# Performance work log

Measured on AMD Instinct MI355X. Metric: run time of the kernel, lower is better.

The kernel has to match this reference:

```python
import jax, jax.numpy as jnp
import numpy as np

# Quantization / threshold constants (from init_kwargs)
AQI, AQF = 8, 8      # activation fixed-point: int/frac bits
NQI, NQF = 2, 8      # nonlinearity output fixed-point
TH_X = 0.1           # delta threshold on input
TH_H = 0.1           # delta threshold on hidden state


def _round_ste(x):
    # straight-through round (GradPreserveRoundTensor in the original util)
    return x + jax.lax.stop_gradient(jnp.round(x) - x)


def quantize(x, qi, qf):
    # util.quantize_tensor with quantize=1: fake-quantize to Q(qi).(qf) fixed point
    power = jnp.asarray(2.0 ** qf, x.dtype)
    clip_val = 2.0 ** (qi + qf - 1)
    return jnp.clip(_round_ste(x * power), -clip_val, clip_val - 1) / power


def setup_inputs() -> dict:
    key = jax.random.key(0)
    k0, k1, k2, k3, k4 = jax.random.split(key, 5)
    T, B, I, H = 512, 64, 512, 1024
    G = 4 * H
    return {
        "x": jax.random.normal(k0, (T, B, I), jnp.float32),
        "weight_ih": jax.random.normal(k1, (G, I), jnp.float32) / np.sqrt(I).astype(np.float32),
        "weight_hh": jax.random.normal(k2, (G, H), jnp.float32) / np.sqrt(H).astype(np.float32),
        "bias_ih": jax.random.normal(k3, (G,), jnp.float32) * 0.1,
        "bias_hh": jax.random.normal(k4, (G,), jnp.float32) * 0.1,
    }


def reference(x, weight_ih, weight_hh, bias_ih, bias_hh):
    T, B, I = x.shape
    H = weight_hh.shape[1]
    dt = x.dtype

    th_x_q = quantize(jnp.asarray(TH_X, dt), AQI, AQF)  # quantized threshold for delta mask
    th_h_q = quantize(jnp.asarray(TH_H, dt), AQI, AQF)

    xs = quantize(x, AQI, AQF)  # inputs quantized once up front

    # initial state (initialize_state with state=None)
    x_prev0 = jnp.zeros((B, I), dt)           # Q(zeros) == zeros
    h0 = jnp.zeros((B, H), dt)
    hp0 = jnp.zeros((B, H), dt)
    c0 = jnp.zeros((B, H), dt)
    m0 = jnp.zeros((B, 4 * H), dt) + bias_ih + bias_hh  # biases folded into m once
    reg0 = jnp.zeros((), dt)

    w_ih_t = weight_ih.T  # [I, 4H]
    w_hh_t = weight_hh.T  # [H, 4H]

    def step(carry, x_t):
        x_prev, h, h_prev, c, m, reg = carry
        dx = x_t - x_prev
        dh = h - h_prev
        dxa = jnp.abs(dx)
        dha = jnp.abs(dh)
        dx = jnp.where(dxa < th_x_q, jnp.asarray(0, dt), dx)   # masked_fill with quantized th
        dh = jnp.where(dha < th_h_q, jnp.asarray(0, dt), dh)
        x_prev = jnp.where(dxa >= TH_X, x_t, x_prev)           # state update with raw th (as in source)
        h_prev = jnp.where(dha >= TH_H, h, h_prev)
        reg = reg + jnp.sum(jnp.abs(dh))                       # l1 norm of masked delta_h

        m = dx @ w_ih_t + dh @ w_hh_t + m                      # delta-GEMM accumulated into m
        pre = quantize(m, AQI, AQF)
        p_i, p_f, p_g, p_o = jnp.split(pre, 4, axis=1)
        g_i = quantize(jax.nn.sigmoid(p_i), NQI, NQF)
        g_f = quantize(jax.nn.sigmoid(p_f), NQI, NQF)
        g_o = quantize(jax.nn.sigmoid(p_o), NQI, NQF)
        g_g = quantize(jnp.tanh(p_g), NQI, NQF)

        c_new = c * g_f + g_i * g_g
        q_c = quantize(c_new, AQI, AQF)
        c_tanh = quantize(jnp.tanh(q_c), NQI, NQF)
        h_new = quantize(g_o * c_tanh, AQI, AQF)
        return (x_prev, h_new, h_prev, q_c, m, reg), h_new

    (x_prev, h, h_prev, c, m, reg), out = jax.lax.scan(
        step, (x_prev0, h0, hp0, c0, m0, reg0), xs)

    # x_prev_out is padded to [B, max(I, H)] (zeros beyond input_size)
    x_prev_out = jnp.zeros((B, max(I, H)), dt).at[:, :I].set(x_prev)
    # state tensors stacked over layers (num_layers=1)
    state = (x_prev_out[None], h[None], h_prev[None], c[None], m[None])
    return (out, *state, reg.reshape(1))
```

## Files before the change

kernel.cpp:

```cpp
#include <hip/hip_runtime.h>
#include <hip/hip_fp16.h>
#include <stdint.h>

typedef unsigned short ushort_t;
typedef unsigned int uint_t;
typedef unsigned long long ull_t;
typedef _Float16 half8 __attribute__((ext_vector_type(8)));
typedef float f32x4 __attribute__((ext_vector_type(4)));

#define TSTEPS 512
#define BATCH  64
#define ISZ    512
#define HSZ    1024
#define GSZ    4096
#define NB     256
#define NTH    1024
#define DHFRAG 65536

static constexpr size_t OFF_XPREV = (size_t)TSTEPS * BATCH * HSZ;
static constexpr size_t OFF_H     = OFF_XPREV + (size_t)BATCH * 1024;
static constexpr size_t OFF_HP    = OFF_H  + (size_t)BATCH * HSZ;
static constexpr size_t OFF_C     = OFF_HP + (size_t)BATCH * HSZ;
static constexpr size_t OFF_M     = OFF_C  + (size_t)BATCH * HSZ;
static constexpr size_t OFF_REG   = OFF_M  + (size_t)BATCH * GSZ;

#define TH_RAW 0.1f
#define TH_QNT 0.1015625f

__device__ __forceinline__ float qA(float x) {
  float v = rintf(x * 256.0f);
  v = fminf(fmaxf(v, -32768.0f), 32767.0f);
  return v * 0.00390625f;
}
__device__ __forceinline__ float qN(float x) {
  float v = rintf(x * 256.0f);
  v = fminf(fmaxf(v, -512.0f), 511.0f);
  return v * 0.00390625f;
}
__device__ __forceinline__ float sigm(float x) { return 1.0f / (1.0f + expf(-x)); }

__global__ __launch_bounds__(256) void xscan_kernel(const float* __restrict__ x,
                                                    __half* __restrict__ dx16,
                                                    float* __restrict__ out_xprev) {
  const int gid = blockIdx.x * blockDim.x + threadIdx.x;
  float xp = 0.0f;
  #pragma unroll 8
  for (int t = 0; t < TSTEPS; t++) {
    float xq = qA(x[(size_t)t * (BATCH * ISZ) + gid]);
    float d  = xq - xp;
    float da = fabsf(d);
    dx16[(size_t)t * (BATCH * ISZ) + gid] = __float2half((da < TH_QNT) ? 0.0f : d);
    if (da >= TH_RAW) xp = xq;
  }
  const int b = gid >> 9;
  const int i = gid & 511;
  out_xprev[(size_t)b * 1024 + i]       = xp;
  out_xprev[(size_t)b * 1024 + 512 + i] = 0.0f;
}

__device__ __forceinline__ void gbar_arrive(int* flags, int e) {
  asm volatile("s_waitcnt vmcnt(0)" ::: "memory");
  __syncthreads();
  if (threadIdx.x == 0) {
    __hip_atomic_store(&flags[blockIdx.x], e, __ATOMIC_RELAXED, __HIP_MEMORY_SCOPE_AGENT);
  }
}
__device__ __forceinline__ void gbar_wait(int* flags, int e) {
  if (threadIdx.x < 64) {
    const ull_t* f64 = (const ull_t*)flags;
    const int l = threadIdx.x;
    bool done;
    do {
      ull_t a = __hip_atomic_load(f64 + l,      __ATOMIC_RELAXED, __HIP_MEMORY_SCOPE_AGENT);
      ull_t c = __hip_atomic_load(f64 + 64 + l, __ATOMIC_RELAXED, __HIP_MEMORY_SCOPE_AGENT);
      bool ok = ((int)a >= e) & ((int)(a >> 32) >= e) &
                ((int)c >= e) & ((int)(c >> 32) >= e);
      done = __all(ok);
      if (!done) __builtin_amdgcn_s_sleep(2);
    } while (!done);
  }
  __syncthreads();
}

__global__ __launch_bounds__(NTH, 4) void scan_kernel(
    const __half* __restrict__ dx16, const float* __restrict__ w_ih,
    const float* __restrict__ w_hh, const float* __restrict__ b_ih,
    const float* __restrict__ b_hh, float* __restrict__ out,
    __half* __restrict__ dh16, float* __restrict__ partials, int* flags) {
  __shared__ __align__(16) unsigned char dxbuf[2][65536];
  __shared__ float part[4][64][17];
  __shared__ float red[256];

  const int tid  = threadIdx.x;
  const int wid  = tid >> 6;
  const int lane = tid & 63;
  const int bt   = wid >> 2;
  const int kg   = wid & 3;
  const int lr   = lane & 15;
  const int lq   = lane >> 4;
  const int lkb  = lq * 16;
  const int jb   = (blockIdx.x & 7) * 32 + (blockIdx.x >> 3);

  const int wrow = jb * 4 + (lr & 3) + (lr >> 2) * HSZ;
  half8 wx[4], wh[8];
  #pragma unroll
  for (int kt = 0; kt < 4; ++kt) {
    const float* p = w_ih + (size_t)wrow * ISZ + kg * 128 + kt * 32 + lq * 8;
    half8 v;
    #pragma unroll
    for (int e = 0; e < 8; ++e) v[e] = (_Float16)p[e];
    wx[kt] = v;
  }
  #pragma unroll
  for (int kt = 0; kt < 8; ++kt) {
    const float* p = w_hh + (size_t)wrow * HSZ + kg * 256 + kt * 32 + lq * 8;
    half8 v;
    #pragma unroll
    for (int e = 0; e < 8; ++e) v[e] = (_Float16)p[e];
    wh[kt] = v;
  }

  const int jj = tid & 3;
  const int cb = tid >> 2;
  const int j  = jb * 4 + jj;
  const int g0 = j, g1 = j + HSZ, g2 = j + 2 * HSZ, g3 = j + 3 * HSZ;
  float m0 = 0.f, m1 = 0.f, m2 = 0.f, m3 = 0.f;
  float c = 0.0f, hp = 0.0f, h = 0.0f, regacc = 0.0f;
  if (tid < 256) {
    m0 = b_ih[g0] + b_hh[g0];
    m1 = b_ih[g1] + b_hh[g1];
    m2 = b_ih[g2] + b_hh[g2];
    m3 = b_ih[g3] + b_hh[g3];
  }
  const size_t dhcell2 = ((size_t)(jb >> 1) * 64 + cb) * 2 + (jb & 1);

  const int arow = bt * 16 + lr;
  const int akey = (arow & 7) << 4;
  const int kc0  = kg * 32 + lq;

  {
    const ull_t* __restrict__ sx = (const ull_t*)dx16;
    #pragma unroll
    for (int i = 0; i < 8; ++i) {
      ull_t v = sx[i * 1024 + tid];
      const int u = i * 1024 + tid;
      const int row = u >> 7, cc = u & 127;
      *(ull_t*)(&dxbuf[0][0] + row * 1024 + ((cc * 8) ^ ((row & 7) << 4))) = v;
    }
  }
  __syncthreads();

  f32x4 acc = {0.f, 0.f, 0.f, 0.f};
  {
    const unsigned char* xbase = &dxbuf[0][0] + arow * 1024;
    #pragma unroll
    for (int kt = 0; kt < 4; ++kt) {
      const int col = kg * 256 + kt * 64 + lkb;
      union { uint4 u; half8 hv; } U;
      U.u = *(const uint4*)(xbase + (col ^ akey));
      acc = __builtin_amdgcn_mfma_f32_16x16x32_f16(U.hv, wx[kt], acc, 0, 0, 0);
    }
  }

  for (int t = 0; t < TSTEPS; t++) {
    gbar_wait(flags, t);

    const ull_t* __restrict__ hb = (const ull_t*)(dh16 + (size_t)(t & 1) * DHFRAG);
    ull_t lo[8], hi[8];
    #pragma unroll
    for (int kt = 0; kt < 8; ++kt) {
      const size_t ci = ((size_t)(kc0 + kt * 4) * 64 + arow) * 2;
      lo[kt] = __hip_atomic_load(hb + ci,     __ATOMIC_RELAXED, __HIP_MEMORY_SCOPE_AGENT);
      hi[kt] = __hip_atomic_load(hb + ci + 1, __ATOMIC_RELAXED, __HIP_MEMORY_SCOPE_AGENT);
    }
    #pragma unroll
    for (int kt = 0; kt < 8; ++kt) {
      union { ull_t u[2]; half8 hv; } U;
      U.u[0] = lo[kt]; U.u[1] = hi[kt];
      acc = __builtin_amdgcn_mfma_f32_16x16x32_f16(U.hv, wh[kt], acc, 0, 0, 0);
    }

    #pragma unroll
    for (int r = 0; r < 4; ++r)
      part[kg][bt * 16 + lq * 4 + r][lr] = acc[r];
    __syncthreads();

    if (tid < 256) {
      float s0 = 0.f, s1 = 0.f, s2 = 0.f, s3 = 0.f;
      #pragma unroll
      for (int k2 = 0; k2 < 4; ++k2) {
        s0 += part[k2][cb][jj];
        s1 += part[k2][cb][4 + jj];
        s2 += part[k2][cb][8 + jj];
        s3 += part[k2][cb][12 + jj];
      }
      m0 += s0; m1 += s1; m2 += s2; m3 += s3;

      float pi = qA(m0), pf = qA(m1), pg = qA(m2), po = qA(m3);
      float gi = qN(sigm(pi));
      float gf = qN(sigm(pf));
      float gg = qN(tanhf(pg));
      float go = qN(sigm(po));
      float cn = c * gf + gi * gg;
      c = qA(cn);
      float ct = qN(tanhf(c));
      h = qA(go * ct);

      if (t < TSTEPS - 1) {
        float d  = h - hp;
        float da = fabsf(d);
        float dm = (da < TH_QNT) ? 0.0f : d;
        if (da >= TH_RAW) hp = h;
        regacc += fabsf(dm);
        ushort_t my = __half_as_ushort(__float2half(dm));
        int v1 = __shfl((int)my, lane + 1, 64);
        int v2 = __shfl((int)my, lane + 2, 64);
        int v3 = __shfl((int)my, lane + 3, 64);
        if (jj == 0) {
          ull_t dw = (ull_t)my | ((ull_t)(ushort_t)v1 << 16) |
                     ((ull_t)(ushort_t)v2 << 32) | ((ull_t)(ushort_t)v3 << 48);
          ull_t* dhw = (ull_t*)(dh16 + (size_t)((t + 1) & 1) * DHFRAG);
          __hip_atomic_store(dhw + dhcell2, dw,
                             __ATOMIC_RELAXED, __HIP_MEMORY_SCOPE_AGENT);
        }
      }
    }

    gbar_arrive(flags, t + 1);

    if (tid < 256)
      out[(size_t)t * (BATCH * HSZ) + (size_t)cb * HSZ + j] = h;

    if (t + 1 < TSTEPS) {
      {
        const ull_t* __restrict__ sx =
            (const ull_t*)(dx16 + (size_t)(t + 1) * (BATCH * ISZ));
        unsigned char* dst = &dxbuf[(t + 1) & 1][0];
        #pragma unroll
        for (int i = 0; i < 8; ++i) {
          ull_t v = sx[i * 1024 + tid];
          const int u = i * 1024 + tid;
          const int row = u >> 7, cc = u & 127;
          *(ull_t*)(dst + row * 1024 + ((cc * 8) ^ ((row & 7) << 4))) = v;
        }
      }
      __syncthreads();
      {
        acc = (f32x4){0.f, 0.f, 0.f, 0.f};
        const unsigned char* xbase = &dxbuf[(t + 1) & 1][0] + arow * 1024;
        #pragma unroll
        for (int kt = 0; kt < 4; ++kt) {
          const int col = kg * 256 + kt * 64 + lkb;
          union { uint4 u; half8 hv; } U;
          U.u = *(const uint4*)(xbase + (col ^ akey));
          acc = __builtin_amdgcn_mfma_f32_16x16x32_f16(U.hv, wx[kt], acc, 0, 0, 0);
        }
      }
    }
  }

  if (tid < 256) {
    out[OFF_H  + (size_t)cb * HSZ + j] = h;
    out[OFF_HP + (size_t)cb * HSZ + j] = hp;
    out[OFF_C  + (size_t)cb * HSZ + j] = c;
    out[OFF_M  + (size_t)cb * GSZ + g0] = m0;
    out[OFF_M  + (size_t)cb * GSZ + g1] = m1;
    out[OFF_M  + (size_t)cb * GSZ + g2] = m2;
    out[OFF_M  + (size_t)cb * GSZ + g3] = m3;
  }

  if (tid < 256) red[tid] = regacc;
  __syncthreads();
  for (int s = 128; s > 0; s >>= 1) {
    if (tid < s) red[tid] += red[tid + s];
    __syncthreads();
  }
  if (tid == 0)
    __hip_atomic_store(&partials[blockIdx.x], red[0], __ATOMIC_RELAXED, __HIP_MEMORY_SCOPE_AGENT);
  gbar_arrive(flags, TSTEPS + 1);
  gbar_wait(flags, TSTEPS + 1);
  if (blockIdx.x == 0) {
    if (tid < 256)
      red[tid] = __hip_atomic_load(&partials[tid], __ATOMIC_RELAXED, __HIP_MEMORY_SCOPE_AGENT);
    __syncthreads();
    for (int s = 128; s > 0; s >>= 1) {
      if (tid < s) red[tid] += red[tid + s];
      __syncthreads();
    }
    if (tid == 0) out[OFF_REG] = red[0];
  }
}

extern "C" void kernel_launch(void* const* d_in, const int* in_sizes, int n_in,
                              void* d_out, int out_size, void* d_ws, size_t ws_size,
                              hipStream_t stream) {
  const float* x    = (const float*)d_in[0];
  const float* w_ih = (const float*)d_in[1];
  const float* w_hh = (const float*)d_in[2];
  const float* b_ih = (const float*)d_in[3];
  const float* b_hh = (const float*)d_in[4];
  float* out = (float*)d_out;

  const size_t dx_elems = (size_t)TSTEPS * BATCH * ISZ;
  __half* dx16     = (__half*)d_ws;
  __half* dh16     = dx16 + dx_elems;
  float*  partials = (float*)(dh16 + 2 * (size_t)DHFRAG);
  int*    flags    = (int*)(partials + NB);
  size_t needed = (size_t)((char*)(flags + NB) - (char*)d_ws);
  if (ws_size < needed) return;

  (void)hipMemsetAsync(dh16, 0, 2 * (size_t)DHFRAG * sizeof(__half), stream);
  (void)hipMemsetAsync(flags, 0, NB * sizeof(int), stream);
  xscan_kernel<<<128, 256, 0, stream>>>(x, dx16, out + OFF_XPREV);
  scan_kernel<<<NB, NTH, 0, stream>>>(dx16, w_ih, w_hh, b_ih, b_hh, out,
                                      dh16, partials, flags);
}
```

Baseline: 2.898 ms.

## Replace global barrier with per-wave partial flag waits and restructure step schedule

Each wave now polls only the 64 producer flags for the k-slice of dh it consumes, instead of every block waiting for all 256 flags. Each block publishes its own flag after a vmcnt drain and a block barrier. The dx-GEMM part is moved after the wait and overlapped with the dh loads, and the next step's dx tile is staged before a trailing syncthreads. A separate flag array serves the final reduction barrier. The aim is to cut inter-block barrier latency on the recurrent critical path, at the risk of memory-ordering subtleties with relaxed atomics.

```diff
diff --git a/kernel.cpp b/kernel.cpp
--- a/kernel.cpp
+++ b/kernel.cpp
@@ -86,7 +86,8 @@
     const __half* __restrict__ dx16, const float* __restrict__ w_ih,
     const float* __restrict__ w_hh, const float* __restrict__ b_ih,
     const float* __restrict__ b_hh, float* __restrict__ out,
-    __half* __restrict__ dh16, float* __restrict__ partials, int* flags) {
+    __half* __restrict__ dh16, float* __restrict__ partials,
+    int* flags, int* flagsE) {
   __shared__ __align__(16) unsigned char dxbuf[2][65536];
   __shared__ float part[4][64][17];
   __shared__ float red[256];
@@ -137,6 +138,7 @@
   const int arow = bt * 16 + lr;
   const int akey = (arow & 7) << 4;
   const int kc0  = kg * 32 + lq;
+  const int fidx = kg * 32 + (lane & 31);
 
   {
     const ull_t* __restrict__ sx = (const ull_t*)dx16;
@@ -150,20 +152,17 @@
   }
   __syncthreads();
 
-  f32x4 acc = {0.f, 0.f, 0.f, 0.f};
-  {
-    const unsigned char* xbase = &dxbuf[0][0] + arow * 1024;
-    #pragma unroll
-    for (int kt = 0; kt < 4; ++kt) {
-      const int col = kg * 256 + kt * 64 + lkb;
-      union { uint4 u; half8 hv; } U;
-      U.u = *(const uint4*)(xbase + (col ^ akey));
-      acc = __builtin_amdgcn_mfma_f32_16x16x32_f16(U.hv, wx[kt], acc, 0, 0, 0);
-    }
-  }
-
   for (int t = 0; t < TSTEPS; t++) {
-    gbar_wait(flags, t);
+    {
+      const ull_t* f64 = (const ull_t*)flags;
+      bool done;
+      do {
+        ull_t v = __hip_atomic_load(f64 + fidx, __ATOMIC_RELAXED, __HIP_MEMORY_SCOPE_AGENT);
+        done = __all(((int)v >= t) & ((int)(v >> 32) >= t));
+        if (!done) __builtin_amdgcn_s_sleep(1);
+      } while (!done);
+      asm volatile("" ::: "memory");
+    }
 
     const ull_t* __restrict__ hb = (const ull_t*)(dh16 + (size_t)(t & 1) * DHFRAG);
     ull_t lo[8], hi[8];
@@ -172,6 +171,18 @@
       const size_t ci = ((size_t)(kc0 + kt * 4) * 64 + arow) * 2;
       lo[kt] = __hip_atomic_load(hb + ci,     __ATOMIC_RELAXED, __HIP_MEMORY_SCOPE_AGENT);
       hi[kt] = __hip_atomic_load(hb + ci + 1, __ATOMIC_RELAXED, __HIP_MEMORY_SCOPE_AGENT);
+    }
+
+    f32x4 acc = {0.f, 0.f, 0.f, 0.f};
+    {
+      const unsigned char* xbase = &dxbuf[t & 1][0] + arow * 1024;
+      #pragma unroll
+      for (int kt = 0; kt < 4; ++kt) {
+        const int col = kg * 256 + kt * 64 + lkb;
+        union { uint4 u; half8 hv; } U;
+        U.u = *(const uint4*)(xbase + (col ^ akey));
+        acc = __builtin_amdgcn_mfma_f32_16x16x32_f16(U.hv, wx[kt], acc, 0, 0, 0);
+      }
     }
     #pragma unroll
     for (int kt = 0; kt < 8; ++kt) {
@@ -226,37 +237,26 @@
       }
     }
 
-    gbar_arrive(flags, t + 1);
+    asm volatile("s_waitcnt vmcnt(0)" ::: "memory");
+    __syncthreads();
+    if (tid == 0)
+      __hip_atomic_store(&flags[jb], t + 1, __ATOMIC_RELAXED, __HIP_MEMORY_SCOPE_AGENT);
 
     if (tid < 256)
       out[(size_t)t * (BATCH * HSZ) + (size_t)cb * HSZ + j] = h;
-
     if (t + 1 < TSTEPS) {
-      {
-        const ull_t* __restrict__ sx =
-            (const ull_t*)(dx16 + (size_t)(t + 1) * (BATCH * ISZ));
-        unsigned char* dst = &dxbuf[(t + 1) & 1][0];
-        #pragma unroll
-        for (int i = 0; i < 8; ++i) {
-          ull_t v = sx[i * 1024 + tid];
-          const int u = i * 1024 + tid;
-          const int row = u >> 7, cc = u & 127;
-          *(ull_t*)(dst + row * 1024 + ((cc * 8) ^ ((row & 7) << 4))) = v;
-        }
+      const ull_t* __restrict__ sx =
+          (const ull_t*)(dx16 + (size_t)(t + 1) * (BATCH * ISZ));
+      unsigned char* dst = &dxbuf[(t + 1) & 1][0];
+      #pragma unroll
+      for (int i = 0; i < 8; ++i) {
+        ull_t v = sx[i * 1024 + tid];
+        const int u = i * 1024 + tid;
+        const int row = u >> 7, cc = u & 127;
+        *(ull_t*)(dst + row * 1024 + ((cc * 8) ^ ((row & 7) << 4))) = v;
       }
-      __syncthreads();
-      {
-        acc = (f32x4){0.f, 0.f, 0.f, 0.f};
-        const unsigned char* xbase = &dxbuf[(t + 1) & 1][0] + arow * 1024;
-        #pragma unroll
-        for (int kt = 0; kt < 4; ++kt) {
-          const int col = kg * 256 + kt * 64 + lkb;
-          union { uint4 u; half8 hv; } U;
-          U.u = *(const uint4*)(xbase + (col ^ akey));
-          acc = __builtin_amdgcn_mfma_f32_16x16x32_f16(U.hv, wx[kt], acc, 0, 0, 0);
-        }
-      }
-    }
+    }
+    __syncthreads();
   }
 
   if (tid < 256) {
@@ -277,8 +277,8 @@
   }
   if (tid == 0)
     __hip_atomic_store(&partials[blockIdx.x], red[0], __ATOMIC_RELAXED, __HIP_MEMORY_SCOPE_AGENT);
-  gbar_arrive(flags, TSTEPS + 1);
-  gbar_wait(flags, TSTEPS + 1);
+  gbar_arrive(flagsE, 1);
+  gbar_wait(flagsE, 1);
   if (blockIdx.x == 0) {
     if (tid < 256)
       red[tid] = __hip_atomic_load(&partials[tid], __ATOMIC_RELAXED, __HIP_MEMORY_SCOPE_AGENT);
@@ -306,12 +306,13 @@
   __half* dh16     = dx16 + dx_elems;
   float*  partials = (float*)(dh16 + 2 * (size_t)DHFRAG);
   int*    flags    = (int*)(partials + NB);
-  size_t needed = (size_t)((char*)(flags + NB) - (char*)d_ws);
+  int*    flagsE   = flags + NB;
+  size_t needed = (size_t)((char*)(flagsE + NB) - (char*)d_ws);
   if (ws_size < needed) return;
 
   (void)hipMemsetAsync(dh16, 0, 2 * (size_t)DHFRAG * sizeof(__half), stream);
-  (void)hipMemsetAsync(flags, 0, NB * sizeof(int), stream);
+  (void)hipMemsetAsync(flags, 0, 2 * NB * sizeof(int), stream);
   xscan_kernel<<<128, 256, 0, stream>>>(x, dx16, out + OFF_XPREV);
   scan_kernel<<<NB, NTH, 0, stream>>>(dx16, w_ih, w_hh, b_ih, b_hh, out,
-                                      dh16, partials, flags);
-}
+                                      dh16, partials, flags, flagsE);
+}
```

New measurement: 3.023 ms. 4.3% more time.
